# Optimization experiments

Measured on AMD Instinct MI355X. Metric: run time of the kernel, lower is better.

The kernel has to match this reference:

```python
import jax, jax.numpy as jnp
import numpy as np

KH = KW = 3
STRIDE = 1
PAD = 1
DIL = 1
DG = 1  # deformable groups


def setup_inputs() -> dict:
    key = jax.random.key(0)
    k1, k2, k3, k4 = jax.random.split(key, 4)
    B, C, H, W = 8, 256, 64, 64
    OC = 256
    x = jax.random.normal(k1, (B, C, H, W), dtype=jnp.float32)
    offset = jax.random.normal(k2, (B, 2 * DG * KH * KW, H, W), dtype=jnp.float32)
    mask = jax.random.uniform(k3, (B, DG * KH * KW, H, W), dtype=jnp.float32)
    stdv = 1.0 / np.sqrt(C * KH * KW)
    weight = jax.random.uniform(k4, (OC, C, KH, KW), dtype=jnp.float32, minval=-stdv, maxval=stdv)
    bias = jnp.zeros((OC,), dtype=jnp.float32)
    return {"x": x, "offset": offset, "mask": mask, "weight": weight, "bias": bias}


def _deform_sample(x, py, px):
    """Bilinear sample x (B,C,H,W) at fractional locations py/px (B,K,Ho,Wo),
    zero outside the image. Returns (B,C,K,Ho,Wo)."""
    B, C, H, W = x.shape
    xf = x.reshape(B, C, H * W)
    y0 = jnp.floor(py)
    x0 = jnp.floor(px)
    wy1 = py - y0
    wx1 = px - x0

    def corner(yc, xc, w):
        valid = (yc >= 0) & (yc < H) & (xc >= 0) & (xc < W)
        yi = jnp.clip(yc, 0, H - 1).astype(jnp.int32)
        xi = jnp.clip(xc, 0, W - 1).astype(jnp.int32)
        idx = (yi * W + xi).reshape(B, -1)  # (B, K*Ho*Wo)
        g = jax.vmap(lambda xb, ib: xb[:, ib])(xf, idx)  # (B,C,K*Ho*Wo)
        g = g.reshape(B, C, *yc.shape[1:])
        return g * (w * valid)[:, None]

    return (
        corner(y0, x0, (1 - wy1) * (1 - wx1))
        + corner(y0, x0 + 1, (1 - wy1) * wx1)
        + corner(y0 + 1, x0, wy1 * (1 - wx1))
        + corner(y0 + 1, x0 + 1, wy1 * wx1)
    )


def reference(x, offset, mask, weight, bias):
    B, C, H, W = x.shape
    OC = weight.shape[0]
    K = KH * KW
    Ho = (H + 2 * PAD - DIL * (KH - 1) - 1) // STRIDE + 1
    Wo = (W + 2 * PAD - DIL * (KW - 1) - 1) // STRIDE + 1

    # base sampling grid: top-left anchor + kernel taps
    oy = jnp.arange(Ho, dtype=jnp.float32) * STRIDE - PAD  # (Ho,)
    ox = jnp.arange(Wo, dtype=jnp.float32) * STRIDE - PAD  # (Wo,)
    ky = jnp.repeat(jnp.arange(KH, dtype=jnp.float32) * DIL, KW)  # (K,)
    kx = jnp.tile(jnp.arange(KW, dtype=jnp.float32) * DIL, KH)    # (K,)

    # offsets: channels laid out as (dg, k, [dy, dx]); dg == 1 here
    off = offset.reshape(B, DG, K, 2, Ho, Wo)
    py = ky[None, :, None, None] + oy[None, None, :, None] + off[:, 0, :, 0]  # (B,K,Ho,Wo)
    px = kx[None, :, None, None] + ox[None, None, None, :] + off[:, 0, :, 1]

    cols = _deform_sample(x, py, px)  # (B,C,K,Ho,Wo)
    cols = cols * mask.reshape(B, 1, K, Ho, Wo)  # modulation

    out = jnp.einsum('bckhw,ock->bohw', cols, weight.reshape(OC, C, K))
    return out + bias[None, :, None, None]
```

## Files before the change

kernel.cpp:

```cpp
#include <hip/hip_runtime.h>
#include <stdint.h>


typedef __attribute__((ext_vector_type(8))) _Float16 half8;
typedef __attribute__((ext_vector_type(2))) __fp16 fp16x2;
typedef __attribute__((ext_vector_type(4))) float floatx4;
typedef __attribute__((ext_vector_type(4))) unsigned int uintx4;

#define MFMA16(A, B, C) __builtin_amdgcn_mfma_f32_16x16x32_f16(A, B, C, 0, 0, 0)

__device__ __forceinline__ unsigned short f16_bits_rne(float v) {
    _Float16 hf = (_Float16)v;
    union { _Float16 f; unsigned short s; } a; a.f = hf;
    return a.s;
}

__device__ __forceinline__ void pack8(const float* vals, uintx4& pkH) {
#pragma unroll
    for (int p = 0; p < 4; p++) {
        fp16x2 h = __builtin_amdgcn_cvt_pkrtz(vals[2 * p], vals[2 * p + 1]);
        union { fp16x2 v; unsigned int u; } ch; ch.v = h;
        pkH[p] = ch.u;
    }
}

__device__ __forceinline__ void mk_coords(int tap, int ho, int wo,
    float offy, float offx, float m,
    int& yx00, int& yx01, int& yx10, int& yx11,
    float& w00, float& w01, float& w10, float& w11) {
    float py = (float)(tap / 3) + (float)(ho - 1) + offy;
    float px = (float)(tap % 3) + (float)(wo - 1) + offx;
    float y0f = floorf(py), x0f = floorf(px);
    float wy1 = py - y0f, wx1 = px - x0f;
    float wy0 = 1.f - wy1, wx0 = 1.f - wx1;
    int y0 = (int)y0f, x0 = (int)x0f, y1 = y0 + 1, x1 = x0 + 1;
    bool vy0 = (y0 >= 0) && (y0 < 64), vy1 = (y1 >= 0) && (y1 < 64);
    bool vx0 = (x0 >= 0) && (x0 < 64), vx1 = (x1 >= 0) && (x1 < 64);
    int cy0 = min(max(y0, 0), 63), cy1 = min(max(y1, 0), 63);
    int cx0 = min(max(x0, 0), 63), cx1 = min(max(x1, 0), 63);
    yx00 = cy0 * 64 + cx0; yx01 = cy0 * 64 + cx1;
    yx10 = cy1 * 64 + cx0; yx11 = cy1 * 64 + cx1;
    w00 = wy0 * wx0 * m * ((vy0 && vx0) ? 1.f : 0.f);
    w01 = wy0 * wx1 * m * ((vy0 && vx1) ? 1.f : 0.f);
    w10 = wy1 * wx0 * m * ((vy1 && vx0) ? 1.f : 0.f);
    w11 = wy1 * wx1 * m * ((vy1 && vx1) ? 1.f : 0.f);
}

__global__ __launch_bounds__(256) void k_prep(const float* __restrict__ x,
                                              const float* __restrict__ w,
                                              unsigned short* __restrict__ xtfh,
                                              unsigned short* __restrict__ bw2) {
    __shared__ float T[64][65];
    const int blk = blockIdx.x;
    const int t = threadIdx.x;
    if (blk < 2048) {
        const int b = blk >> 8;
        const int ct = (blk >> 6) & 3;
        const int tt = blk & 63;
        const int jj = t & 63, i4 = t >> 6;
        const float* xb = x + ((size_t)b << 20);
#pragma unroll 4
        for (int ii = 0; ii < 16; ii++) {
            int i = ii * 4 + i4;
            T[i][jj] = xb[((size_t)(ct * 64 + i) << 12) + tt * 64 + jj];
        }
        __syncthreads();
        unsigned short* ob = xtfh + ((size_t)b << 20);
#pragma unroll 4
        for (int ii = 0; ii < 16; ii++) {
            int jo = ii * 4 + i4;
            ob[((size_t)(tt * 64 + jo) << 8) + ct * 64 + jj] = f16_bits_rne(T[jj][jo]);
        }
    } else {
        int tid = (blk - 2048) * 256 + t;
        int j = tid & 7;
        int oc = (tid >> 3) & 255;
        int c = (tid >> 11) & 3;
        int step = tid >> 13;
        int ktap = step >> 3;
        int ch = ((step & 7) << 5) + (c << 3) + j;
        float v = w[oc * 2304 + ch * 9 + ktap] * 64.f;
        bw2[tid] = f16_bits_rne(v);
    }
}

__global__ __launch_bounds__(512, 4) void k_dcn_v14(
    const float* __restrict__ offset,
    const float* __restrict__ mask,
    const float* __restrict__ bias,
    const unsigned short* __restrict__ xtfh,
    const unsigned short* __restrict__ bw2,
    float* __restrict__ out)
{
    __shared__ __align__(16) unsigned short Bs[9 * 2112];

    const int t = threadIdx.x;
    const int tile = blockIdx.x;
    const int b = tile & 7;
    const int ho = tile >> 3;

    const int lane = t & 63, w8 = t >> 6, quad = (t >> 4) & 3, l15 = t & 15;
    const int grp = t >> 8;
    const int th = t & 255;
    const int gpos = th >> 2, gseg = th & 3;
    const int wo = gpos;
    const int spos = (ho << 6) + wo;
    const unsigned short* xh = xtfh + ((size_t)b << 20);

    const unsigned short* aBase = bw2 + quad * 2048 + (((w8 << 5) + l15) << 3);

    floatx4 acc[2][4];
#pragma unroll
    for (int i = 0; i < 2; i++)
#pragma unroll
        for (int j = 0; j < 4; j++) acc[i][j] = (floatx4){0.f, 0.f, 0.f, 0.f};

    float om0s[5], om1s[5], omms[5];
#pragma unroll
    for (int s = 0; s < 5; ++s) {
        int tap = 2 * s + grp; if (tap > 8) tap = 8;
        om0s[s] = offset[((size_t)(b * 18 + 2 * tap) << 12) + spos];
        om1s[s] = offset[((size_t)(b * 18 + 2 * tap + 1) << 12) + spos];
        omms[s] = mask[((size_t)(b * 9 + tap) << 12) + spos];
    }

    half8 aCur[2], aNxt[2];
    half8 crnA[4], crnB[4];
    int yxs[2][4];
    float wss[2][4];

#define MK(S, SET) do { int _tap = 2 * (S) + grp; if (_tap > 8) _tap = 8;   \
    mk_coords(_tap, ho, wo, om0s[S], om1s[S], omms[S],                      \
        yxs[SET][0], yxs[SET][1], yxs[SET][2], yxs[SET][3],                 \
        wss[SET][0], wss[SET][1], wss[SET][2], wss[SET][3]); } while (0)

#define LOAD_CRN(DST, SET, C) do {                                          \
    const int cb = ((C) << 5) + (gseg << 3);                                \
    DST[0] = *(const half8*)(xh + ((size_t)yxs[SET][0] << 8) + cb);         \
    DST[1] = *(const half8*)(xh + ((size_t)yxs[SET][1] << 8) + cb);         \
    DST[2] = *(const half8*)(xh + ((size_t)yxs[SET][2] << 8) + cb);         \
    DST[3] = *(const half8*)(xh + ((size_t)yxs[SET][3] << 8) + cb);         \
    } while (0)

#define GEN_WRITE(CRN, SET, SLOT) do {                                      \
    float vals[8];                                                          \
    _Pragma("unroll")                                                       \
    for (int q = 0; q < 8; q++) {                                           \
        vals[q] = wss[SET][0] * (float)CRN[0][q]                            \
                + wss[SET][1] * (float)CRN[1][q]                            \
                + wss[SET][2] * (float)CRN[2][q]                            \
                + wss[SET][3] * (float)CRN[3][q];                           \
    }                                                                       \
    uintx4 pkH;                                                             \
    pack8(vals, pkH);                                                       \
    unsigned short* bp = Bs + (SLOT) * 2112 + gseg * 528 + (gpos << 3);     \
    *(uintx4*)bp = pkH;                                                     \
    } while (0)

#define LOAD_A(DST, STEP) do {                                              \
    const unsigned short* ap = aBase + (size_t)(STEP) * 8192;               \
    DST[0] = *(const half8*)ap;                                             \
    DST[1] = *(const half8*)(ap + 128);                                     \
    } while (0)

#define MFMA_STEP(SLOT, AREG) do {                                          \
    const unsigned short* Bp = Bs + (SLOT) * 2112 + quad * 528;             \
    half8 bH[4];                                                            \
    _Pragma("unroll")                                                       \
    for (int j = 0; j < 4; j++)                                             \
        bH[j] = *(const half8*)(Bp + (((j << 4) + l15) << 3));              \
    _Pragma("unroll")                                                       \
    for (int i = 0; i < 2; i++)                                             \
    _Pragma("unroll")                                                       \
        for (int j = 0; j < 4; j++)                                         \
            acc[i][j] = MFMA16(AREG[i], bH[j], acc[i][j]);                  \
    } while (0)

    for (int c = 0; c < 8; ++c) {
        MK(0, 0);
        LOAD_CRN(crnA, 0, c);
#pragma unroll
        for (int s = 0; s < 5; ++s) {
            if (s < 4) {
                if ((s & 1) == 0) { MK(s + 1, 1); LOAD_CRN(crnB, 1, c); }
                else              { MK(s + 1, 0); LOAD_CRN(crnA, 0, c); }
            }
            const int slot = 2 * s + grp;
            if (s < 4 || grp == 0) {
                if ((s & 1) == 0) GEN_WRITE(crnA, 0, slot);
                else              GEN_WRITE(crnB, 1, slot);
            }
        }
        __syncthreads();

        LOAD_A(aCur, c);
#pragma unroll
        for (int tp = 0; tp < 9; ++tp) {
            if (tp < 8) {
                if ((tp & 1) == 0) LOAD_A(aNxt, (tp + 1) * 8 + c);
                else               LOAD_A(aCur, (tp + 1) * 8 + c);
            }
            if ((tp & 1) == 0) MFMA_STEP(tp, aCur);
            else               MFMA_STEP(tp, aNxt);
        }
        __syncthreads();
    }

    float* outb = out + ((size_t)b << 20);
    const int posbase = ho << 6;
#pragma unroll
    for (int i = 0; i < 2; i++) {
        const int ocb = (w8 << 5) + (i << 4) + (quad << 2);
#pragma unroll
        for (int r = 0; r < 4; r++) {
            const float bv = bias[ocb + r];
#pragma unroll
            for (int j = 0; j < 4; j++) {
                const int pos = posbase + (j << 4) + l15;
                outb[((size_t)(ocb + r) << 12) + pos] = acc[i][j][r] * 0.015625f + bv;
            }
        }
    }
#undef MK
#undef LOAD_CRN
#undef GEN_WRITE
#undef LOAD_A
#undef MFMA_STEP
}

__device__ __forceinline__ void split_f16_bits(float v, unsigned int& h, unsigned int& l) {
    _Float16 hf = (_Float16)v;
    float hff = (float)hf;
    _Float16 lf = (_Float16)(v - hff);
    union { _Float16 f; unsigned short s; } a2, b2;
    a2.f = hf; b2.f = lf;
    h = a2.s; l = b2.s;
}
__device__ __forceinline__ void split_pack8(const float* vals, uintx4& pkH, uintx4& pkL) {
#pragma unroll
    for (int p = 0; p < 4; p++) {
        float v0 = vals[2 * p], v1 = vals[2 * p + 1];
        fp16x2 h = __builtin_amdgcn_cvt_pkrtz(v0, v1);
        float h0 = (float)h[0], h1 = (float)h[1];
        fp16x2 l = __builtin_amdgcn_cvt_pkrtz(v0 - h0, v1 - h1);
        union { fp16x2 v; unsigned int u; } ch, cl;
        ch.v = h; cl.v = l;
        pkH[p] = ch.u;
        pkL[p] = cl.u;
    }
}

__global__ __launch_bounds__(256, 2) void k_dcn_fb(
    const float* __restrict__ x, const float* __restrict__ offset,
    const float* __restrict__ mask, const float* __restrict__ weight,
    const float* __restrict__ bias, float* __restrict__ out)
{
    __shared__ __align__(16) unsigned short AsH[256 * 40];
    __shared__ __align__(16) unsigned short AsL[256 * 40];
    __shared__ __align__(16) unsigned short BsH[64 * 40];
    __shared__ __align__(16) unsigned short BsL[64 * 40];
    __shared__ int cY[64][4];
    __shared__ float cW[64][4];

    const int t = threadIdx.x;
    const int tile = blockIdx.x;
    const int b = tile >> 6;
    const int ho = tile & 63;
    const int lane = t & 63, wid = t >> 6, quad = lane >> 4, l15 = lane & 15;
    const int gpos = t >> 2, gseg = t & 3;

    floatx4 acc[4][4];
#pragma unroll
    for (int i = 0; i < 4; i++)
#pragma unroll
        for (int j = 0; j < 4; j++) acc[i][j] = (floatx4){0.f, 0.f, 0.f, 0.f};

    for (int ktap = 0; ktap < 9; ++ktap) {
        __syncthreads();
        if (t < 64) {
            int wo = t;
            int spos = (ho << 6) + wo;
            float offy = offset[(((size_t)(b * 18 + 2 * ktap)) << 12) + spos];
            float offx = offset[(((size_t)(b * 18 + 2 * ktap + 1)) << 12) + spos];
            float m = mask[(((size_t)(b * 9 + ktap)) << 12) + spos];
            int c0, c1, c2, c3; float u0, u1, u2, u3;
            mk_coords(ktap, ho, wo, offy, offx, m, c0, c1, c2, c3, u0, u1, u2, u3);
            cY[t][0] = c0; cY[t][1] = c1; cY[t][2] = c2; cY[t][3] = c3;
            cW[t][0] = u0; cW[t][1] = u1; cW[t][2] = u2; cW[t][3] = u3;
        }
        __syncthreads();
        const int yx00 = cY[gpos][0], yx01 = cY[gpos][1];
        const int yx10 = cY[gpos][2], yx11 = cY[gpos][3];
        const float w00 = cW[gpos][0], w01 = cW[gpos][1];
        const float w10 = cW[gpos][2], w11 = cW[gpos][3];

        for (int cs = 0; cs < 8; ++cs) {
            const int c0 = cs << 5;
            {
                const float* wp = weight + (size_t)t * 2304 + (size_t)c0 * 9 + ktap;
#pragma unroll
                for (int kj = 0; kj < 32; kj += 2) {
                    unsigned int h0, l0u, h1, l1u;
                    split_f16_bits(wp[kj * 9] * 64.f, h0, l0u);
                    split_f16_bits(wp[kj * 9 + 9] * 64.f, h1, l1u);
                    *(unsigned int*)&AsH[t * 40 + kj] = h0 | (h1 << 16);
                    *(unsigned int*)&AsL[t * 40 + kj] = l0u | (l1u << 16);
                }
            }
            {
                const int cb = c0 + (gseg << 3);
                const float* xg = x + ((size_t)b << 20);
                float vals[8];
#pragma unroll
                for (int j = 0; j < 8; j++) {
                    const float* xc = xg + ((size_t)(cb + j) << 12);
                    vals[j] = w00 * xc[yx00] + w01 * xc[yx01] +
                              w10 * xc[yx10] + w11 * xc[yx11];
                }
                uintx4 pkH, pkL;
                split_pack8(vals, pkH, pkL);
                *(uintx4*)&BsH[gpos * 40 + (gseg << 3)] = pkH;
                *(uintx4*)&BsL[gpos * 40 + (gseg << 3)] = pkL;
            }
            __syncthreads();
            half8 aH[4], aL[4], bH[4], bL[4];
#pragma unroll
            for (int i = 0; i < 4; i++) {
                const int rowA = (wid << 6) + (i << 4) + l15;
                aH[i] = *(const half8*)&AsH[rowA * 40 + (quad << 3)];
                aL[i] = *(const half8*)&AsL[rowA * 40 + (quad << 3)];
            }
#pragma unroll
            for (int j = 0; j < 4; j++) {
                const int rowB = (j << 4) + l15;
                bH[j] = *(const half8*)&BsH[rowB * 40 + (quad << 3)];
                bL[j] = *(const half8*)&BsL[rowB * 40 + (quad << 3)];
            }
#pragma unroll
            for (int i = 0; i < 4; i++)
#pragma unroll
                for (int j = 0; j < 4; j++) {
                    acc[i][j] = MFMA16(aH[i], bH[j], acc[i][j]);
                    acc[i][j] = MFMA16(aL[i], bH[j], acc[i][j]);
                    acc[i][j] = MFMA16(aH[i], bL[j], acc[i][j]);
                }
            __syncthreads();
        }
    }
    float* outb = out + ((size_t)b << 20);
    const int posbase = ho << 6;
#pragma unroll
    for (int i = 0; i < 4; i++) {
        const int ocb = (wid << 6) + (i << 4) + (quad << 2);
#pragma unroll
        for (int r = 0; r < 4; r++) {
            const float bv = bias[ocb + r];
#pragma unroll
            for (int j = 0; j < 4; j++) {
                const int pos = posbase + (j << 4) + l15;
                outb[((size_t)(ocb + r) << 12) + pos] = acc[i][j][r] * 0.015625f + bv;
            }
        }
    }
}

extern "C" void kernel_launch(void* const* d_in, const int* in_sizes, int n_in,
                              void* d_out, int out_size, void* d_ws, size_t ws_size,
                              hipStream_t stream) {
    const float* x      = (const float*)d_in[0];
    const float* offset = (const float*)d_in[1];
    const float* mask   = (const float*)d_in[2];
    const float* weight = (const float*)d_in[3];
    const float* bias   = (const float*)d_in[4];
    float* out = (float*)d_out;

    const size_t xtf_bytes = (size_t)8 * 4096 * 256 * 2;
    const size_t bw2_elems = (size_t)72 * 8192;
    const size_t need = xtf_bytes + bw2_elems * 2;

    if (ws_size >= need) {
        unsigned short* xtfh = (unsigned short*)d_ws;
        unsigned short* bw2 = (unsigned short*)((char*)d_ws + xtf_bytes);
        k_prep<<<2048 + 2304, 256, 0, stream>>>(x, weight, xtfh, bw2);
        k_dcn_v14<<<512, 512, 0, stream>>>(offset, mask, bias, xtfh, bw2, out);
    } else {
        k_dcn_fb<<<512, 256, 0, stream>>>(x, offset, mask, weight, bias, out);
    }
}
```

Before: 148.0 us.

## Fuse prep and DCN kernels into one cooperative launch with grid sync

Merges the layout/precision prep step (x transpose to fp16 NHWC and weight repack) into the main deformable-conv kernel. Each block first does its share of the prep work using shared memory as a transpose buffer, then a cooperative grid-wide sync precedes the existing gather+MFMA loop. This removes a separate kernel launch and the inter-kernel gap, but adds the cost of a grid barrier and needs all 512 blocks of 512 threads to be co-resident. It falls back to the two-kernel path if the cooperative launch fails.

Result: slower. 229.8 us (+55.2%).

```diff
diff --git a/kernel.cpp b/kernel.cpp
--- a/kernel.cpp
+++ b/kernel.cpp
@@ -1,4 +1,5 @@
 #include <hip/hip_runtime.h>
+#include <hip/hip_cooperative_groups.h>
 #include <stdint.h>
 
 
@@ -46,6 +47,201 @@
     w11 = wy1 * wx1 * m * ((vy1 && vx1) ? 1.f : 0.f);
 }
 
+__global__ __launch_bounds__(512, 4) void k_dcn_v15(
+    const float* __restrict__ x,
+    const float* __restrict__ w,
+    const float* __restrict__ offset,
+    const float* __restrict__ mask,
+    const float* __restrict__ bias,
+    unsigned short* __restrict__ xtfh,
+    unsigned short* __restrict__ bw2,
+    float* __restrict__ out)
+{
+    __shared__ __align__(16) unsigned short Bs[9 * 2112];
+
+    const int t = threadIdx.x;
+    const int tile = blockIdx.x;
+
+    {
+        float* Tf = (float*)Bs;
+        const int grp = t >> 8;
+        const int th = t & 255;
+        const int jj = th & 63, i4 = th >> 6;
+        float* Tg = Tf + grp * (64 * 65);
+#pragma unroll
+        for (int k = 0; k < 2; ++k) {
+            const int job = tile * 4 + grp * 2 + k;
+            const int b = job >> 8;
+            const int ct = (job >> 6) & 3;
+            const int tt = job & 63;
+            const float* xb = x + ((size_t)b << 20);
+            __syncthreads();
+#pragma unroll 4
+            for (int ii = 0; ii < 16; ii++) {
+                int i = ii * 4 + i4;
+                Tg[i * 65 + jj] = xb[((size_t)(ct * 64 + i) << 12) + tt * 64 + jj];
+            }
+            __syncthreads();
+            unsigned short* ob = xtfh + ((size_t)b << 20);
+#pragma unroll 4
+            for (int ii = 0; ii < 16; ii++) {
+                int jo = ii * 4 + i4;
+                ob[((size_t)(tt * 64 + jo) << 8) + ct * 64 + jj] =
+                    f16_bits_rne(Tg[jj * 65 + jo]);
+            }
+        }
+        const int lin = tile * 512 + t;
+#pragma unroll
+        for (int pass = 0; pass < 3; ++pass) {
+            int tid = lin + pass * 262144;
+            if (tid < 589824) {
+                int j = tid & 7;
+                int oc = (tid >> 3) & 255;
+                int c = (tid >> 11) & 3;
+                int step = tid >> 13;
+                int ktap = step >> 3;
+                int ch = ((step & 7) << 5) + (c << 3) + j;
+                float v = w[oc * 2304 + ch * 9 + ktap] * 64.f;
+                bw2[tid] = f16_bits_rne(v);
+            }
+        }
+    }
+
+    cooperative_groups::this_grid().sync();
+
+    const int b = tile & 7;
+    const int ho = tile >> 3;
+
+    const int w8 = t >> 6, quad = (t >> 4) & 3, l15 = t & 15;
+    const int grp = t >> 8;
+    const int th = t & 255;
+    const int gpos = th >> 2, gseg = th & 3;
+    const int wo = gpos;
+    const int spos = (ho << 6) + wo;
+    const unsigned short* xh = xtfh + ((size_t)b << 20);
+
+    const unsigned short* aBase = bw2 + quad * 2048 + (((w8 << 5) + l15) << 3);
+
+    floatx4 acc[2][4];
+#pragma unroll
+    for (int i = 0; i < 2; i++)
+#pragma unroll
+        for (int j = 0; j < 4; j++) acc[i][j] = (floatx4){0.f, 0.f, 0.f, 0.f};
+
+    float om0s[5], om1s[5], omms[5];
+#pragma unroll
+    for (int s = 0; s < 5; ++s) {
+        int tap = 2 * s + grp; if (tap > 8) tap = 8;
+        om0s[s] = offset[((size_t)(b * 18 + 2 * tap) << 12) + spos];
+        om1s[s] = offset[((size_t)(b * 18 + 2 * tap + 1) << 12) + spos];
+        omms[s] = mask[((size_t)(b * 9 + tap) << 12) + spos];
+    }
+
+    half8 aCur[2], aNxt[2];
+    half8 crnA[4], crnB[4];
+    int yxs[2][4];
+    float wss[2][4];
+
+#define MK(S, SET) do { int _tap = 2 * (S) + grp; if (_tap > 8) _tap = 8;   \
+    mk_coords(_tap, ho, wo, om0s[S], om1s[S], omms[S],                      \
+        yxs[SET][0], yxs[SET][1], yxs[SET][2], yxs[SET][3],                 \
+        wss[SET][0], wss[SET][1], wss[SET][2], wss[SET][3]); } while (0)
+
+#define LOAD_CRN(DST, SET, C) do {                                          \
+    const int cb = ((C) << 5) + (gseg << 3);                                \
+    DST[0] = *(const half8*)(xh + ((size_t)yxs[SET][0] << 8) + cb);         \
+    DST[1] = *(const half8*)(xh + ((size_t)yxs[SET][1] << 8) + cb);         \
+    DST[2] = *(const half8*)(xh + ((size_t)yxs[SET][2] << 8) + cb);         \
+    DST[3] = *(const half8*)(xh + ((size_t)yxs[SET][3] << 8) + cb);         \
+    } while (0)
+
+#define GEN_WRITE(CRN, SET, SLOT) do {                                      \
+    float vals[8];                                                          \
+    _Pragma("unroll")                                                       \
+    for (int q = 0; q < 8; q++) {                                           \
+        vals[q] = wss[SET][0] * (float)CRN[0][q]                            \
+                + wss[SET][1] * (float)CRN[1][q]                            \
+                + wss[SET][2] * (float)CRN[2][q]                            \
+                + wss[SET][3] * (float)CRN[3][q];                           \
+    }                                                                       \
+    uintx4 pkH;                                                             \
+    pack8(vals, pkH);                                                       \
+    unsigned short* bp = Bs + (SLOT) * 2112 + gseg * 528 + (gpos << 3);     \
+    *(uintx4*)bp = pkH;                                                     \
+    } while (0)
+
+#define LOAD_A(DST, STEP) do {                                              \
+    const unsigned short* ap = aBase + (size_t)(STEP) * 8192;               \
+    DST[0] = *(const half8*)ap;                                             \
+    DST[1] = *(const half8*)(ap + 128);                                     \
+    } while (0)
+
+#define MFMA_STEP(SLOT, AREG) do {                                          \
+    const unsigned short* Bp = Bs + (SLOT) * 2112 + quad * 528;             \
+    half8 bH[4];                                                            \
+    _Pragma("unroll")                                                       \
+    for (int j = 0; j < 4; j++)                                             \
+        bH[j] = *(const half8*)(Bp + (((j << 4) + l15) << 3));              \
+    _Pragma("unroll")                                                       \
+    for (int i = 0; i < 2; i++)                                             \
+    _Pragma("unroll")                                                       \
+        for (int j = 0; j < 4; j++)                                         \
+            acc[i][j] = MFMA16(AREG[i], bH[j], acc[i][j]);                  \
+    } while (0)
+
+    __syncthreads();
+    for (int c = 0; c < 8; ++c) {
+        MK(0, 0);
+        LOAD_CRN(crnA, 0, c);
+#pragma unroll
+        for (int s = 0; s < 5; ++s) {
+            if (s < 4) {
+                if ((s & 1) == 0) { MK(s + 1, 1); LOAD_CRN(crnB, 1, c); }
+                else              { MK(s + 1, 0); LOAD_CRN(crnA, 0, c); }
+            }
+            const int slot = 2 * s + grp;
+            if (s < 4 || grp == 0) {
+                if ((s & 1) == 0) GEN_WRITE(crnA, 0, slot);
+                else              GEN_WRITE(crnB, 1, slot);
+            }
+        }
+        __syncthreads();
+
+        LOAD_A(aCur, c);
+#pragma unroll
+        for (int tp = 0; tp < 9; ++tp) {
+            if (tp < 8) {
+                if ((tp & 1) == 0) LOAD_A(aNxt, (tp + 1) * 8 + c);
+                else               LOAD_A(aCur, (tp + 1) * 8 + c);
+            }
+            if ((tp & 1) == 0) MFMA_STEP(tp, aCur);
+            else               MFMA_STEP(tp, aNxt);
+        }
+        __syncthreads();
+    }
+
+    float* outb = out + ((size_t)b << 20);
+    const int posbase = ho << 6;
+#pragma unroll
+    for (int i = 0; i < 2; i++) {
+        const int ocb = (w8 << 5) + (i << 4) + (quad << 2);
+#pragma unroll
+        for (int r = 0; r < 4; r++) {
+            const float bv = bias[ocb + r];
+#pragma unroll
+            for (int j = 0; j < 4; j++) {
+                const int pos = posbase + (j << 4) + l15;
+                outb[((size_t)(ocb + r) << 12) + pos] = acc[i][j][r] * 0.015625f + bv;
+            }
+        }
+    }
+#undef MK
+#undef LOAD_CRN
+#undef GEN_WRITE
+#undef LOAD_A
+#undef MFMA_STEP
+}
+
 __global__ __launch_bounds__(256) void k_prep(const float* __restrict__ x,
                                               const float* __restrict__ w,
                                               unsigned short* __restrict__ xtfh,
@@ -99,14 +295,13 @@
     const int b = tile & 7;
     const int ho = tile >> 3;
 
-    const int lane = t & 63, w8 = t >> 6, quad = (t >> 4) & 3, l15 = t & 15;
+    const int w8 = t >> 6, quad = (t >> 4) & 3, l15 = t & 15;
     const int grp = t >> 8;
     const int th = t & 255;
     const int gpos = th >> 2, gseg = th & 3;
     const int wo = gpos;
     const int spos = (ho << 6) + wo;
     const unsigned short* xh = xtfh + ((size_t)b << 20);
-
     const unsigned short* aBase = bw2 + quad * 2048 + (((w8 << 5) + l15) << 3);
 
     floatx4 acc[2][4];
@@ -381,8 +576,16 @@
     if (ws_size >= need) {
         unsigned short* xtfh = (unsigned short*)d_ws;
         unsigned short* bw2 = (unsigned short*)((char*)d_ws + xtf_bytes);
-        k_prep<<<2048 + 2304, 256, 0, stream>>>(x, weight, xtfh, bw2);
-        k_dcn_v14<<<512, 512, 0, stream>>>(offset, mask, bias, xtfh, bw2, out);
+
+        void* args[] = { (void*)&x, (void*)&weight, (void*)&offset,
+                         (void*)&mask, (void*)&bias, (void*)&xtfh,
+                         (void*)&bw2, (void*)&out };
+        hipError_t err = hipLaunchCooperativeKernel(
+            (const void*)k_dcn_v15, dim3(512), dim3(512), args, 0, stream);
+        if (err != hipSuccess) {
+            k_prep<<<2048 + 2304, 256, 0, stream>>>(x, weight, xtfh, bw2);
+            k_dcn_v14<<<512, 512, 0, stream>>>(offset, mask, bias, xtfh, bw2, out);
+        }
     } else {
         k_dcn_fb<<<512, 256, 0, stream>>>(x, offset, mask, weight, bias, out);
     }
```

## Split each output row into two half-row tiles to double block count

Applied to the files above, without the earlier changes.

Each block now covers 32 output positions instead of a full 64-wide row, so the grid grows from 512 to 1024 blocks. The shared B tile shrinks by half. The wave layout changes to 4 OC groups by 2 position groups, each wave holding 4 accumulators instead of 8. The register double-buffering of corner and weight loads is removed and launch bounds rise to 6 waves per SIMD, trading explicit software pipelining for higher occupancy and more parallelism on 256 CUs. The cost is that each weight fragment is reloaded from global memory twice as often, since half as many positions share it.

Result: slower. 215.3 us (+45.4%).

```diff
diff --git a/kernel.cpp b/kernel.cpp
--- a/kernel.cpp
+++ b/kernel.cpp
@@ -84,7 +84,7 @@
     }
 }
 
-__global__ __launch_bounds__(512, 4) void k_dcn_v14(
+__global__ __launch_bounds__(512, 6) void k_dcn_v16(
     const float* __restrict__ offset,
     const float* __restrict__ mask,
     const float* __restrict__ bias,
@@ -92,133 +92,120 @@
     const unsigned short* __restrict__ bw2,
     float* __restrict__ out)
 {
-    __shared__ __align__(16) unsigned short Bs[9 * 2112];
+    __shared__ __align__(16) unsigned short Bs[9 * 1088];
 
     const int t = threadIdx.x;
     const int tile = blockIdx.x;
     const int b = tile & 7;
-    const int ho = tile >> 3;
-
-    const int lane = t & 63, w8 = t >> 6, quad = (t >> 4) & 3, l15 = t & 15;
-    const int grp = t >> 8;
-    const int th = t & 255;
-    const int gpos = th >> 2, gseg = th & 3;
-    const int wo = gpos;
+    const int hp = tile >> 3;
+    const int ho = hp >> 1;
+    const int hh = hp & 1;
+
+    const int w8 = t >> 6;
+    const int ocg = w8 >> 1;
+    const int pg = w8 & 1;
+    const int quad = (t >> 4) & 3, l15 = t & 15;
+
+    const int g = t >> 7;
+    const int th = t & 127;
+    const int gpos = th >> 2;
+    const int gseg = th & 3;
+    const int wo = (hh << 5) + gpos;
     const int spos = (ho << 6) + wo;
     const unsigned short* xh = xtfh + ((size_t)b << 20);
 
-    const unsigned short* aBase = bw2 + quad * 2048 + (((w8 << 5) + l15) << 3);
-
-    floatx4 acc[2][4];
-#pragma unroll
-    for (int i = 0; i < 2; i++)
-#pragma unroll
-        for (int j = 0; j < 4; j++) acc[i][j] = (floatx4){0.f, 0.f, 0.f, 0.f};
-
-    float om0s[5], om1s[5], omms[5];
-#pragma unroll
-    for (int s = 0; s < 5; ++s) {
-        int tap = 2 * s + grp; if (tap > 8) tap = 8;
+    const unsigned short* aBase = bw2 + quad * 2048 + (((ocg << 6) + l15) << 3);
+
+    floatx4 acc[4];
+#pragma unroll
+    for (int i = 0; i < 4; i++) acc[i] = (floatx4){0.f, 0.f, 0.f, 0.f};
+
+    float om0s[3], om1s[3], omms[3];
+#pragma unroll
+    for (int s = 0; s < 3; ++s) {
+        const int tap = (s == 2) ? 8 : (g + (s << 2));
         om0s[s] = offset[((size_t)(b * 18 + 2 * tap) << 12) + spos];
         om1s[s] = offset[((size_t)(b * 18 + 2 * tap + 1) << 12) + spos];
         omms[s] = mask[((size_t)(b * 9 + tap) << 12) + spos];
     }
 
-    half8 aCur[2], aNxt[2];
-    half8 crnA[4], crnB[4];
-    int yxs[2][4];
-    float wss[2][4];
-
-#define MK(S, SET) do { int _tap = 2 * (S) + grp; if (_tap > 8) _tap = 8;   \
+    half8 aC[4];
+    half8 crn[4];
+    int yx[4];
+    float ws[4];
+
+#define MK(S) do { const int _tap = ((S) == 2) ? 8 : (g + ((S) << 2));      \
     mk_coords(_tap, ho, wo, om0s[S], om1s[S], omms[S],                      \
-        yxs[SET][0], yxs[SET][1], yxs[SET][2], yxs[SET][3],                 \
-        wss[SET][0], wss[SET][1], wss[SET][2], wss[SET][3]); } while (0)
-
-#define LOAD_CRN(DST, SET, C) do {                                          \
+        yx[0], yx[1], yx[2], yx[3], ws[0], ws[1], ws[2], ws[3]); } while (0)
+
+#define LOAD_CRN(C) do {                                                    \
     const int cb = ((C) << 5) + (gseg << 3);                                \
-    DST[0] = *(const half8*)(xh + ((size_t)yxs[SET][0] << 8) + cb);         \
-    DST[1] = *(const half8*)(xh + ((size_t)yxs[SET][1] << 8) + cb);         \
-    DST[2] = *(const half8*)(xh + ((size_t)yxs[SET][2] << 8) + cb);         \
-    DST[3] = *(const half8*)(xh + ((size_t)yxs[SET][3] << 8) + cb);         \
+    crn[0] = *(const half8*)(xh + ((size_t)yx[0] << 8) + cb);               \
+    crn[1] = *(const half8*)(xh + ((size_t)yx[1] << 8) + cb);               \
+    crn[2] = *(const half8*)(xh + ((size_t)yx[2] << 8) + cb);               \
+    crn[3] = *(const half8*)(xh + ((size_t)yx[3] << 8) + cb);               \
     } while (0)
 
-#define GEN_WRITE(CRN, SET, SLOT) do {                                      \
+#define GEN_WRITE(SLOT) do {                                                \
     float vals[8];                                                          \
     _Pragma("unroll")                                                       \
     for (int q = 0; q < 8; q++) {                                           \
-        vals[q] = wss[SET][0] * (float)CRN[0][q]                            \
-                + wss[SET][1] * (float)CRN[1][q]                            \
-                + wss[SET][2] * (float)CRN[2][q]                            \
-                + wss[SET][3] * (float)CRN[3][q];                           \
+        vals[q] = ws[0] * (float)crn[0][q] + ws[1] * (float)crn[1][q]       \
+                + ws[2] * (float)crn[2][q] + ws[3] * (float)crn[3][q];      \
     }                                                                       \
     uintx4 pkH;                                                             \
     pack8(vals, pkH);                                                       \
-    unsigned short* bp = Bs + (SLOT) * 2112 + gseg * 528 + (gpos << 3);     \
+    unsigned short* bp = Bs + (SLOT) * 1088 + gseg * 272 + (gpos << 3);     \
     *(uintx4*)bp = pkH;                                                     \
     } while (0)
 
-#define LOAD_A(DST, STEP) do {                                              \
+#define LOAD_A(STEP) do {                                                   \
     const unsigned short* ap = aBase + (size_t)(STEP) * 8192;               \
-    DST[0] = *(const half8*)ap;                                             \
-    DST[1] = *(const half8*)(ap + 128);                                     \
+    aC[0] = *(const half8*)ap;                                              \
+    aC[1] = *(const half8*)(ap + 128);                                      \
+    aC[2] = *(const half8*)(ap + 256);                                      \
+    aC[3] = *(const half8*)(ap + 384);                                      \
     } while (0)
 
-#define MFMA_STEP(SLOT, AREG) do {                                          \
-    const unsigned short* Bp = Bs + (SLOT) * 2112 + quad * 528;             \
-    half8 bH[4];                                                            \
-    _Pragma("unroll")                                                       \
-    for (int j = 0; j < 4; j++)                                             \
-        bH[j] = *(const half8*)(Bp + (((j << 4) + l15) << 3));              \
-    _Pragma("unroll")                                                       \
-    for (int i = 0; i < 2; i++)                                             \
-    _Pragma("unroll")                                                       \
-        for (int j = 0; j < 4; j++)                                         \
-            acc[i][j] = MFMA16(AREG[i], bH[j], acc[i][j]);                  \
+#define MFMA_STEP(SLOT) do {                                                \
+    const unsigned short* Bp = Bs + (SLOT) * 1088 + quad * 272              \
+                             + (pg << 7) + (l15 << 3);                      \
+    const half8 bH = *(const half8*)Bp;                                     \
+    acc[0] = MFMA16(aC[0], bH, acc[0]);                                     \
+    acc[1] = MFMA16(aC[1], bH, acc[1]);                                     \
+    acc[2] = MFMA16(aC[2], bH, acc[2]);                                     \
+    acc[3] = MFMA16(aC[3], bH, acc[3]);                                     \
     } while (0)
 
     for (int c = 0; c < 8; ++c) {
-        MK(0, 0);
-        LOAD_CRN(crnA, 0, c);
-#pragma unroll
-        for (int s = 0; s < 5; ++s) {
-            if (s < 4) {
-                if ((s & 1) == 0) { MK(s + 1, 1); LOAD_CRN(crnB, 1, c); }
-                else              { MK(s + 1, 0); LOAD_CRN(crnA, 0, c); }
-            }
-            const int slot = 2 * s + grp;
-            if (s < 4 || grp == 0) {
-                if ((s & 1) == 0) GEN_WRITE(crnA, 0, slot);
-                else              GEN_WRITE(crnB, 1, slot);
-            }
-        }
-        __syncthreads();
-
-        LOAD_A(aCur, c);
+#pragma unroll
+        for (int s = 0; s < 3; ++s) {
+            if (s < 2 || g == 0) {
+                MK(s);
+                LOAD_CRN(c);
+                GEN_WRITE((s == 2) ? 8 : (g + (s << 2)));
+            }
+        }
+        __syncthreads();
+
 #pragma unroll
         for (int tp = 0; tp < 9; ++tp) {
-            if (tp < 8) {
-                if ((tp & 1) == 0) LOAD_A(aNxt, (tp + 1) * 8 + c);
-                else               LOAD_A(aCur, (tp + 1) * 8 + c);
-            }
-            if ((tp & 1) == 0) MFMA_STEP(tp, aCur);
-            else               MFMA_STEP(tp, aNxt);
+            LOAD_A(tp * 8 + c);
+            MFMA_STEP(tp);
         }
         __syncthreads();
     }
 
     float* outb = out + ((size_t)b << 20);
-    const int posbase = ho << 6;
-#pragma unroll
-    for (int i = 0; i < 2; i++) {
-        const int ocb = (w8 << 5) + (i << 4) + (quad << 2);
+    const int posbase = (ho << 6) + (hh << 5) + (pg << 4);
+#pragma unroll
+    for (int i = 0; i < 4; i++) {
+        const int ocb = (ocg << 6) + (i << 4) + (quad << 2);
 #pragma unroll
         for (int r = 0; r < 4; r++) {
             const float bv = bias[ocb + r];
-#pragma unroll
-            for (int j = 0; j < 4; j++) {
-                const int pos = posbase + (j << 4) + l15;
-                outb[((size_t)(ocb + r) << 12) + pos] = acc[i][j][r] * 0.015625f + bv;
-            }
+            const int pos = posbase + l15;
+            outb[((size_t)(ocb + r) << 12) + pos] = acc[i][r] * 0.015625f + bv;
         }
     }
 #undef MK
@@ -382,7 +369,7 @@
         unsigned short* xtfh = (unsigned short*)d_ws;
         unsigned short* bw2 = (unsigned short*)((char*)d_ws + xtf_bytes);
         k_prep<<<2048 + 2304, 256, 0, stream>>>(x, weight, xtfh, bw2);
-        k_dcn_v14<<<512, 512, 0, stream>>>(offset, mask, bias, xtfh, bw2, out);
+        k_dcn_v16<<<1024, 512, 0, stream>>>(offset, mask, bias, xtfh, bw2, out);
     } else {
         k_dcn_fb<<<512, 256, 0, stream>>>(x, offset, mask, weight, bias, out);
     }
```
